# Kernel optimization log

Measured on AMD Instinct MI355X. Metric: run time of the kernel, lower is better.

## Reference

```python
import jax, jax.numpy as jnp
import numpy as np

B, S, D, H, DFF = 2, 2048, 1024, 16, 4096
DK = D // H
EPS = 1e-6
MASK_FILL = -1.0  # original code uses -1**9 == -1 (precedence bug), NOT -1e9


def layernorm(x, gamma, beta):
    # original: (x - mean) / (std + eps), std unbiased (torch default ddof=1), scalar gamma/beta
    mean = jnp.mean(x, axis=-1, keepdims=True)
    std = jnp.std(x, axis=-1, keepdims=True, ddof=1)
    return gamma * (x - mean) / (std + EPS) + beta


def setup_inputs() -> dict:
    key = jax.random.key(0)
    ks = jax.random.split(key, 12)
    sc = 0.02
    return {
        "x": jax.random.normal(ks[0], (B, S, D), jnp.float32),
        "src_mask": jnp.ones((B, 1, 1, S), jnp.int32),
        "wq": jax.random.normal(ks[1], (D, D), jnp.float32) * sc,
        "bq": jnp.zeros((D,), jnp.float32),
        "wk": jax.random.normal(ks[2], (D, D), jnp.float32) * sc,
        "bk": jnp.zeros((D,), jnp.float32),
        "wv": jax.random.normal(ks[3], (D, D), jnp.float32) * sc,
        "bv": jnp.zeros((D,), jnp.float32),
        "wo": jax.random.normal(ks[4], (D, D), jnp.float32) * sc,
        "bo": jnp.zeros((D,), jnp.float32),
        "w1": jax.random.normal(ks[5], (D, DFF), jnp.float32) * sc,
        "b1": jnp.zeros((DFF,), jnp.float32),
        "w2": jax.random.normal(ks[6], (DFF, D), jnp.float32) * sc,
        "b2": jnp.zeros((D,), jnp.float32),
        "g1": jnp.ones((), jnp.float32),
        "be1": jnp.zeros((), jnp.float32),
        "g2": jnp.ones((), jnp.float32),
        "be2": jnp.zeros((), jnp.float32),
    }


def reference(x, src_mask, wq, bq, wk, bk, wv, bv, wo, bo,
              w1, b1, w2, b2, g1, be1, g2, be2):
    # --- residual 1: pre-LN self-attention ---
    xn = layernorm(x, g1, be1)
    q = (xn @ wq + bq).reshape(B, S, H, DK).transpose(0, 2, 1, 3)  # [B,H,S,DK]
    k = (xn @ wk + bk).reshape(B, S, H, DK).transpose(0, 2, 1, 3)
    v = (xn @ wv + bv).reshape(B, S, H, DK).transpose(0, 2, 1, 3)
    scores = jnp.einsum('bhqd,bhkd->bhqk', q, k) / jnp.sqrt(jnp.float32(DK))
    scores = jnp.where(src_mask == 0, MASK_FILL, scores)
    attn = jax.nn.softmax(scores, axis=-1)
    ctx = jnp.einsum('bhqk,bhkd->bhqd', attn, v)
    ctx = ctx.transpose(0, 2, 1, 3).reshape(B, S, D)
    attn_out = ctx @ wo + bo
    x = x + attn_out  # dropout is identity in eval

    # --- residual 2: pre-LN feed-forward ---
    xn = layernorm(x, g2, be2)
    h = jax.nn.relu(xn @ w1 + b1)
    ff_out = h @ w2 + b2
    return x + ff_out
```

## Files before the change

kernel.cpp:

```cpp
#include <hip/hip_runtime.h>

typedef unsigned short u16;
typedef __bf16 bf16x8 __attribute__((ext_vector_type(8)));
typedef float f32x4 __attribute__((ext_vector_type(4)));

#define AS1U(p) ((__attribute__((address_space(1))) unsigned int*)(p))
#define AS3U(p) ((__attribute__((address_space(3))) unsigned int*)(p))

__device__ __forceinline__ u16 f2bf(float f) {
  union { float f; unsigned int i; } c; c.f = f;
  return (u16)((c.i + 0x7FFFu + ((c.i >> 16) & 1u)) >> 16);
}
__device__ __forceinline__ u16 f2bf_trunc(float f) {
  union { float f; unsigned int i; } c; c.f = f;
  return (u16)(c.i >> 16);
}

template <int BM, int BN, int BK, int OMODE>
__global__ __launch_bounds__(256) void gemm_bt(
    const u16* __restrict__ A, long lda,
    const u16* __restrict__ B, long ldb,
    void* __restrict__ Cv, long ldc,
    int K, float scale, const float* __restrict__ bias,
    const float* __restrict__ res, long ldres, int relu) {
  constexpr int WN = (BN == 128) ? 64 : 32;
  constexpr int MI = 4, NJ = WN / 16;
  constexpr int KK = BK / 32;
  __shared__ u16 As0[BM * BK], As1[BM * BK];
  __shared__ u16 Bs0[BN * BK], Bs1[BN * BK];
  const int t = threadIdx.x;
  const int w = t >> 6, l = t & 63;
  const int wr = w >> 1, wc = w & 1;
  const int quad = l >> 4, mlo = l & 15;
  const long row0 = (long)blockIdx.x * BM;
  const long col0 = (long)blockIdx.y * BN;

  f32x4 acc[MI][NJ] = {};

  auto stage = [&](u16 (&Ad)[BM * BK], u16 (&Bd)[BN * BK], int k0) {
    if (BK == 32) {
#pragma unroll
      for (int i = 0; i < BM / 64; i++) {
        int s = t + i * 256, r = s >> 2, c = s & 3;
        const u16* g = A + (row0 + r) * lda + k0 + c * 8;
        __builtin_amdgcn_global_load_lds(AS1U(g), AS3U(&Ad[s * 8]), 16, 0, 0);
      }
#pragma unroll
      for (int i = 0; i < BN / 64; i++) {
        int s = t + i * 256, r = s >> 2, c = s & 3;
        const u16* g = B + (col0 + r) * ldb + k0 + c * 8;
        __builtin_amdgcn_global_load_lds(AS1U(g), AS3U(&Bd[s * 8]), 16, 0, 0);
      }
    } else {
#pragma unroll
      for (int i = 0; i < BM / 32; i++) {
        int s = t + i * 256, r = s >> 3, c = s & 7;
        const u16* g = A + (row0 + r) * lda + k0 + (c ^ (r & 7)) * 8;
        __builtin_amdgcn_global_load_lds(AS1U(g), AS3U(&Ad[s * 8]), 16, 0, 0);
      }
#pragma unroll
      for (int i = 0; i < BN / 32; i++) {
        int s = t + i * 256, r = s >> 3, c = s & 7;
        const u16* g = B + (col0 + r) * ldb + k0 + (c ^ (r & 7)) * 8;
        __builtin_amdgcn_global_load_lds(AS1U(g), AS3U(&Bd[s * 8]), 16, 0, 0);
      }
    }
  };
  auto compute = [&](const u16 (&Asr)[BM * BK], const u16 (&Bsr)[BN * BK]) {
#pragma unroll
    for (int kk = 0; kk < KK; kk++) {
      bf16x8 a[MI], b[NJ];
#pragma unroll
      for (int i = 0; i < MI; i++) {
        int r = wr * 64 + i * 16 + mlo;
        a[i] = (BK == 32) ? *(const bf16x8*)&Asr[(r * 4 + quad) * 8]
                          : *(const bf16x8*)&Asr[(r * 8 + ((kk * 4 + quad) ^ (r & 7))) * 8];
      }
#pragma unroll
      for (int j = 0; j < NJ; j++) {
        int r = wc * WN + j * 16 + mlo;
        b[j] = (BK == 32) ? *(const bf16x8*)&Bsr[(r * 4 + quad) * 8]
                          : *(const bf16x8*)&Bsr[(r * 8 + ((kk * 4 + quad) ^ (r & 7))) * 8];
      }
#pragma unroll
      for (int i = 0; i < MI; i++)
#pragma unroll
        for (int j = 0; j < NJ; j++)
          acc[i][j] = __builtin_amdgcn_mfma_f32_16x16x32_bf16(a[i], b[j], acc[i][j], 0, 0, 0);
    }
  };

  stage(As0, Bs0, 0);
  for (int k0 = 0; k0 < K; k0 += 2 * BK) {
    __syncthreads();
    stage(As1, Bs1, k0 + BK);
    compute(As0, Bs0);
    __syncthreads();
    if (k0 + 2 * BK < K) stage(As0, Bs0, k0 + 2 * BK);
    compute(As1, Bs1);
  }

#pragma unroll
  for (int i = 0; i < MI; i++) {
#pragma unroll
    for (int j = 0; j < NJ; j++) {
      const long gn = col0 + wc * WN + j * 16 + mlo;
      const float bv = bias ? bias[gn] : 0.0f;
#pragma unroll
      for (int r = 0; r < 4; r++) {
        const long gm = row0 + wr * 64 + i * 16 + quad * 4 + r;
        float v = acc[i][j][r] * scale + bv;
        if (relu && v < 0.0f) v = 0.0f;
        if (res) v += res[gm * ldres + gn];
        if (OMODE == 0) ((float*)Cv)[gm * ldc + gn] = v;
        else ((u16*)Cv)[gm * ldc + gn] = f2bf(v);
      }
    }
  }
}

__global__ __launch_bounds__(256) void flash_attn(
    const u16* __restrict__ QKV, const u16* __restrict__ VT,
    const int* __restrict__ mask, u16* __restrict__ ctx) {
  __shared__ u16 Ks[2][64 * 64];
  __shared__ u16 Vs[2][64 * 64];
  __shared__ u16 Ps[128 * 64];
  const int t = threadIdx.x;
  const int w = t >> 6, l = t & 63;
  const int quad = l >> 4, mlo = l & 15;
  const int z = blockIdx.z, b = z >> 4, h = z & 15;
  const long q0 = (long)blockIdx.x * 128;
  const u16* Qg = QKV + (long)b * (2048L * 3072) + h * 64;
  const u16* Kg = Qg + 1024;
  const u16* Vg = VT + (long)b * (1024L * 2048) + (long)(h * 64) * 2048;
  const int* mrow = mask + b * 2048;

#pragma unroll
  for (int i = 0; i < 2; i++) {
    int s = t + i * 256, r = s >> 3, c = s & 7;
    __builtin_amdgcn_global_load_lds(AS1U(Kg + (long)r * 3072 + (c ^ (r & 7)) * 8),
                                     AS3U(&Ks[0][s * 8]), 16, 0, 0);
    __builtin_amdgcn_global_load_lds(AS1U(Vg + (long)r * 2048 + (c ^ (r & 7)) * 8),
                                     AS3U(&Vs[0][s * 8]), 16, 0, 0);
  }
  bf16x8 aq[2][2];
#pragma unroll
  for (int i = 0; i < 2; i++)
#pragma unroll
    for (int kk = 0; kk < 2; kk++) {
      const u16* g = Qg + (q0 + w * 32 + i * 16 + mlo) * 3072 + kk * 32 + quad * 8;
      union { uint4 u; bf16x8 v; } c; c.u = *(const uint4*)g;
      aq[i][kk] = c.v;
    }

  f32x4 o[2][5] = {};
  union { u16 s[8]; bf16x8 v; } ones;
#pragma unroll
  for (int e = 0; e < 8; e++) ones.s[e] = 0x3F80;
  const float CS = 0.125f * 1.44269504f;
  const float CM = -1.44269504f;

  for (int it = 0; it < 32; ++it) {
    const int cur = it & 1;
    const int key0 = it * 64;
    __syncthreads();
    if (it + 1 < 32) {
      const int nb = 1 - cur;
      const u16* Kg2 = Kg + (long)(it + 1) * 64 * 3072;
      const u16* Vg2 = Vg + (it + 1) * 64;
#pragma unroll
      for (int i2 = 0; i2 < 2; i2++) {
        int s = t + i2 * 256, r = s >> 3, c = s & 7;
        __builtin_amdgcn_global_load_lds(AS1U(Kg2 + (long)r * 3072 + (c ^ (r & 7)) * 8),
                                         AS3U(&Ks[nb][s * 8]), 16, 0, 0);
        __builtin_amdgcn_global_load_lds(AS1U(Vg2 + (long)r * 2048 + (c ^ (r & 7)) * 8),
                                         AS3U(&Vs[nb][s * 8]), 16, 0, 0);
      }
    }
    int mz[4];
#pragma unroll
    for (int j = 0; j < 4; j++) mz[j] = mrow[key0 + j * 16 + mlo];
    f32x4 sa[2][4] = {};
#pragma unroll
    for (int kk = 0; kk < 2; kk++) {
      bf16x8 bk[4];
#pragma unroll
      for (int j = 0; j < 4; j++) {
        int rr = j * 16 + mlo;
        bk[j] = *(const bf16x8*)&Ks[cur][(rr * 8 + ((kk * 4 + quad) ^ (mlo & 7))) * 8];
      }
#pragma unroll
      for (int i = 0; i < 2; i++)
#pragma unroll
        for (int j = 0; j < 4; j++)
          sa[i][j] = __builtin_amdgcn_mfma_f32_16x16x32_bf16(aq[i][kk], bk[j], sa[i][j], 0, 0, 0);
    }
#pragma unroll
    for (int i = 0; i < 2; i++) {
      const int rbase = w * 32 + i * 16 + quad * 4;
      const int skey = (rbase >> 2) & 7;
#pragma unroll
      for (int j = 0; j < 4; j++) {
        const int col = j * 16 + mlo;
        u16* pp = &Ps[rbase * 64 + (((col >> 3) ^ skey) << 3) + (col & 7)];
#pragma unroll
        for (int r = 0; r < 4; r++) {
          float s = (mz[j] == 0) ? CM : sa[i][j][r] * CS;
          pp[r * 64] = f2bf_trunc(__builtin_amdgcn_exp2f(s));
        }
      }
    }
#pragma unroll
    for (int kk = 0; kk < 2; kk++) {
      bf16x8 ap[2], bv[4];
#pragma unroll
      for (int i = 0; i < 2; i++) {
        const int row = w * 32 + i * 16 + mlo;
        const int skey = (row >> 2) & 7;
        ap[i] = *(const bf16x8*)&Ps[(row * 8 + ((kk * 4 + quad) ^ skey)) * 8];
      }
#pragma unroll
      for (int j = 0; j < 4; j++) {
        int rr = j * 16 + mlo;
        bv[j] = *(const bf16x8*)&Vs[cur][(rr * 8 + ((kk * 4 + quad) ^ (mlo & 7))) * 8];
      }
#pragma unroll
      for (int i = 0; i < 2; i++) {
#pragma unroll
        for (int j = 0; j < 4; j++)
          o[i][j] = __builtin_amdgcn_mfma_f32_16x16x32_bf16(ap[i], bv[j], o[i][j], 0, 0, 0);
        o[i][4] = __builtin_amdgcn_mfma_f32_16x16x32_bf16(ap[i], ones.v, o[i][4], 0, 0, 0);
      }
    }
  }
  u16* cb = ctx + (long)b * (2048L * 1024) + q0 * 1024 + h * 64;
#pragma unroll
  for (int i = 0; i < 2; i++)
#pragma unroll
    for (int r = 0; r < 4; r++) {
      float inv = 1.0f / o[i][4][r];
      int row = w * 32 + i * 16 + quad * 4 + r;
#pragma unroll
      for (int j = 0; j < 4; j++)
        cb[(long)row * 1024 + j * 16 + mlo] = f2bf(o[i][j][r] * inv);
    }
}

__device__ __forceinline__ void ln_row(const float* __restrict__ x, u16* __restrict__ y,
                                       const float* __restrict__ g, const float* __restrict__ b,
                                       long row, float* ss, float* s2) {
  const float* xr = x + row * 1024;
  float v[4];
  float s = 0.f, sq = 0.f;
#pragma unroll
  for (int i = 0; i < 4; i++) {
    float f = xr[threadIdx.x + i * 256];
    v[i] = f; s += f; sq += f * f;
  }
#pragma unroll
  for (int o = 32; o > 0; o >>= 1) { s += __shfl_xor(s, o, 64); sq += __shfl_xor(sq, o, 64); }
  const int w = threadIdx.x >> 6;
  if ((threadIdx.x & 63) == 0) { ss[w] = s; s2[w] = sq; }
  __syncthreads();
  s = ss[0] + ss[1] + ss[2] + ss[3];
  sq = s2[0] + s2[1] + s2[2] + s2[3];
  const float mean = s * (1.0f / 1024.0f);
  float var = (sq - s * mean) * (1.0f / 1023.0f);
  var = fmaxf(var, 0.0f);
  const float sc = g[0] / (sqrtf(var) + 1e-6f);
  const float be = b[0];
#pragma unroll
  for (int i = 0; i < 4; i++)
    y[row * 1024 + threadIdx.x + i * 256] = f2bf((v[i] - mean) * sc + be);
}

__global__ __launch_bounds__(256) void ln_kernel(const float* __restrict__ x, u16* __restrict__ y,
                                                 const float* __restrict__ g, const float* __restrict__ b) {
  __shared__ float ss[4], s2[4];
  ln_row(x, y, g, b, blockIdx.x, ss, s2);
}

__global__ __launch_bounds__(256) void prep_kernel(
    const float* __restrict__ x, const float* __restrict__ g1, const float* __restrict__ be1,
    const float* __restrict__ wq, const float* __restrict__ wk, const float* __restrict__ wv,
    const float* __restrict__ wo, const float* __restrict__ w1, const float* __restrict__ w2,
    const float* __restrict__ bq, const float* __restrict__ bk, const float* __restrict__ bv,
    u16* __restrict__ xnH, u16* __restrict__ WqkvT, u16* __restrict__ woT,
    u16* __restrict__ w1T, u16* __restrict__ w2T, float* __restrict__ biasQKV) {
  __shared__ float tile[32][33];
  __shared__ float ss[4], s2[4];
  const int bid = blockIdx.x;
  if (bid >= 12300) {
    ln_row(x, xnH, g1, be1, bid - 12300, ss, s2);
    return;
  }
  if (bid >= 12288) {
    const int i = (bid - 12288) * 256 + threadIdx.x;
    if (i < 3072) biasQKV[i] = (i < 1024) ? bq[i] : ((i < 2048) ? bk[i - 1024] : bv[i - 2048]);
    return;
  }
  const float* in; u16* out; long ldin, ldo; int ti, tiles_x;
  if (bid < 1024)      { in = wq; out = WqkvT;                     ldin = 1024; ldo = 1024; ti = bid;        tiles_x = 32; }
  else if (bid < 2048) { in = wk; out = WqkvT + (size_t)1024*1024; ldin = 1024; ldo = 1024; ti = bid - 1024; tiles_x = 32; }
  else if (bid < 3072) { in = wv; out = WqkvT + (size_t)2048*1024; ldin = 1024; ldo = 1024; ti = bid - 2048; tiles_x = 32; }
  else if (bid < 4096) { in = wo; out = woT;                       ldin = 1024; ldo = 1024; ti = bid - 3072; tiles_x = 32; }
  else if (bid < 8192) { in = w1; out = w1T;                       ldin = 4096; ldo = 1024; ti = bid - 4096; tiles_x = 128; }
  else                 { in = w2; out = w2T;                       ldin = 1024; ldo = 4096; ti = bid - 8192; tiles_x = 32; }
  const int bx = (ti % tiles_x) * 32, by = (ti / tiles_x) * 32;
  const int tx = threadIdx.x & 31, ty = threadIdx.x >> 5;
#pragma unroll
  for (int i = 0; i < 32; i += 8) tile[ty + i][tx] = in[(long)(by + ty + i) * ldin + bx + tx];
  __syncthreads();
#pragma unroll
  for (int i = 0; i < 32; i += 8)
    out[(long)(bx + ty + i) * ldo + by + tx] = f2bf(tile[tx][ty + i]);
}

__global__ __launch_bounds__(256) void ttrans1(const u16* __restrict__ in, long ldin, long siz,
                                               u16* __restrict__ out, long ldo, long soz) {
  __shared__ u16 tile[32][33];
  const long zi = (long)blockIdx.z * siz, zo = (long)blockIdx.z * soz;
  const int bx = blockIdx.x * 32, by = blockIdx.y * 32;
  const int tx = threadIdx.x & 31, ty = threadIdx.x >> 5;
#pragma unroll
  for (int i = 0; i < 32; i += 8)
    tile[ty + i][tx] = in[zi + (long)(by + ty + i) * ldin + bx + tx];
  __syncthreads();
#pragma unroll
  for (int i = 0; i < 32; i += 8)
    out[zo + (long)(bx + ty + i) * ldo + by + tx] = tile[tx][ty + i];
}

extern "C" void kernel_launch(void* const* d_in, const int* in_sizes, int n_in,
                              void* d_out, int out_size, void* d_ws, size_t ws_size,
                              hipStream_t stream) {
  const float* x   = (const float*)d_in[0];
  const int*   msk = (const int*)d_in[1];
  const float* wq  = (const float*)d_in[2];
  const float* bq  = (const float*)d_in[3];
  const float* wk  = (const float*)d_in[4];
  const float* bk  = (const float*)d_in[5];
  const float* wv  = (const float*)d_in[6];
  const float* bv  = (const float*)d_in[7];
  const float* wo  = (const float*)d_in[8];
  const float* bo  = (const float*)d_in[9];
  const float* w1  = (const float*)d_in[10];
  const float* b1  = (const float*)d_in[11];
  const float* w2  = (const float*)d_in[12];
  const float* b2  = (const float*)d_in[13];
  const float* g1  = (const float*)d_in[14];
  const float* be1 = (const float*)d_in[15];
  const float* g2  = (const float*)d_in[16];
  const float* be2 = (const float*)d_in[17];
  float* out = (float*)d_out;

  char* basep = (char*)d_ws;
  size_t off = 0;
  auto au = [&](size_t nelem) -> u16* {
    u16* r = (u16*)(basep + off);
    off += ((nelem * 2) + 255) & ~(size_t)255;
    return r;
  };
  auto afp = [&](size_t nelem) -> float* {
    float* r = (float*)(basep + off);
    off += ((nelem * 4) + 255) & ~(size_t)255;
    return r;
  };

  u16* xnH  = au((size_t)4096 * 1024);
  u16* QKV  = au((size_t)4096 * 3072);
  u16* VTH  = au((size_t)2 * 1024 * 2048);
  u16* ctxH = au((size_t)4096 * 1024);
  float* x1 = afp((size_t)4096 * 1024);
  u16* hb   = au((size_t)4096 * 4096);
  u16* WqkvT = au((size_t)3072 * 1024);
  u16* woT  = au((size_t)1024 * 1024);
  u16* w1T  = au((size_t)4096 * 1024);
  u16* w2T  = au((size_t)1024 * 4096);
  float* biasQKV = afp(3072);

  const dim3 blk(256);

  prep_kernel<<<16396, blk, 0, stream>>>(x, g1, be1, wq, wk, wv, wo, w1, w2,
                                         bq, bk, bv, xnH, WqkvT, woT, w1T, w2T, biasQKV);

  gemm_bt<128, 128, 32, 2><<<dim3(32, 24), blk, 0, stream>>>(
      xnH, 1024, WqkvT, 1024, QKV, 3072, 1024, 1.0f,
      biasQKV, (const float*)0, 0, 0);

  ttrans1<<<dim3(32, 64, 2), blk, 0, stream>>>(
      QKV + 2048, 3072, (long)2048 * 3072, VTH, 2048, (long)1024 * 2048);

  flash_attn<<<dim3(16, 1, 32), blk, 0, stream>>>(QKV, VTH, msk, ctxH);

  gemm_bt<128, 64, 64, 0><<<dim3(32, 16), blk, 0, stream>>>(
      ctxH, 1024, woT, 1024, x1, 1024, 1024, 1.0f, bo, x, 1024, 0);

  ln_kernel<<<4096, blk, 0, stream>>>(x1, xnH, g2, be2);

  gemm_bt<128, 128, 32, 2><<<dim3(32, 32), blk, 0, stream>>>(
      xnH, 1024, w1T, 1024, hb, 4096, 1024, 1.0f,
      b1, (const float*)0, 0, 1);

  gemm_bt<128, 64, 64, 0><<<dim3(32, 16), blk, 0, stream>>>(
      hb, 4096, w2T, 4096, out, 1024, 4096, 1.0f, b2, x1, 1024, 0);
}
```

Before: 366.5 us.

## Split attention key range across two blocks and combine partial results

The flash attention kernel now splits the 2048 keys into two halves over a new grid dimension. Each block writes unnormalized fp32 output partials and softmax denominators instead of final bf16 context. A new combine kernel sums the two partials, divides by the summed denominators and writes the bf16 context. This doubles the number of attention blocks to improve CU occupancy and latency hiding. In exchange it adds an extra launch and roughly 32 MB of fp32 partial writes and reads, with the partials buffer reusing the FFN hidden buffer.

```diff
diff --git a/kernel.cpp b/kernel.cpp
--- a/kernel.cpp
+++ b/kernel.cpp
@@ -121,7 +121,8 @@
 
 __global__ __launch_bounds__(256) void flash_attn(
     const u16* __restrict__ QKV, const u16* __restrict__ VT,
-    const int* __restrict__ mask, u16* __restrict__ ctx) {
+    const int* __restrict__ mask, float* __restrict__ opart,
+    float* __restrict__ denp) {
   __shared__ u16 Ks[2][64 * 64];
   __shared__ u16 Vs[2][64 * 64];
   __shared__ u16 Ps[128 * 64];
@@ -129,11 +130,12 @@
   const int w = t >> 6, l = t & 63;
   const int quad = l >> 4, mlo = l & 15;
   const int z = blockIdx.z, b = z >> 4, h = z & 15;
+  const int y = blockIdx.y;
   const long q0 = (long)blockIdx.x * 128;
   const u16* Qg = QKV + (long)b * (2048L * 3072) + h * 64;
-  const u16* Kg = Qg + 1024;
-  const u16* Vg = VT + (long)b * (1024L * 2048) + (long)(h * 64) * 2048;
-  const int* mrow = mask + b * 2048;
+  const u16* Kg = Qg + 1024 + (long)y * 1024 * 3072;
+  const u16* Vg = VT + (long)b * (1024L * 2048) + (long)(h * 64) * 2048 + y * 1024;
+  const int* mrow = mask + b * 2048 + y * 1024;
 
 #pragma unroll
   for (int i = 0; i < 2; i++) {
@@ -160,11 +162,11 @@
   const float CS = 0.125f * 1.44269504f;
   const float CM = -1.44269504f;
 
-  for (int it = 0; it < 32; ++it) {
+  for (int it = 0; it < 16; ++it) {
     const int cur = it & 1;
     const int key0 = it * 64;
     __syncthreads();
-    if (it + 1 < 32) {
+    if (it + 1 < 16) {
       const int nb = 1 - cur;
       const u16* Kg2 = Kg + (long)(it + 1) * 64 * 3072;
       const u16* Vg2 = Vg + (it + 1) * 64;
@@ -233,17 +235,32 @@
       }
     }
   }
-  u16* cb = ctx + (long)b * (2048L * 1024) + q0 * 1024 + h * 64;
+  float* ob = opart + ((long)(y * 32 + z)) * (2048L * 64) + q0 * 64;
+  float* db = denp + ((long)(y * 32 + z)) * 2048 + q0;
 #pragma unroll
   for (int i = 0; i < 2; i++)
 #pragma unroll
     for (int r = 0; r < 4; r++) {
-      float inv = 1.0f / o[i][4][r];
-      int row = w * 32 + i * 16 + quad * 4 + r;
+      const int row = w * 32 + i * 16 + quad * 4 + r;
 #pragma unroll
       for (int j = 0; j < 4; j++)
-        cb[(long)row * 1024 + j * 16 + mlo] = f2bf(o[i][j][r] * inv);
-    }
+        ob[(long)row * 64 + j * 16 + mlo] = o[i][j][r];
+      if (mlo == 0) db[row] = o[i][4][r];
+    }
+}
+
+__global__ __launch_bounds__(256) void fcombine(
+    const float* __restrict__ opart, const float* __restrict__ denp,
+    u16* __restrict__ ctx) {
+  const long e = (long)blockIdx.x * 256 + threadIdx.x;
+  const long PL = 32L * 2048 * 64;
+  const float o0 = opart[e], o1 = opart[e + PL];
+  const int z = (int)(e >> 17);
+  const int rem = (int)(e & 131071);
+  const int q = rem >> 6, d = rem & 63;
+  const float dn = denp[(long)z * 2048 + q] + denp[(long)(32 + z) * 2048 + q];
+  const int b = z >> 4, h = z & 15;
+  ctx[(long)b * (2048L * 1024) + (long)q * 1024 + h * 64 + d] = f2bf((o0 + o1) / dn);
 }
 
 __device__ __forceinline__ void ln_row(const float* __restrict__ x, u16* __restrict__ y,
@@ -378,6 +395,8 @@
   u16* w1T  = au((size_t)4096 * 1024);
   u16* w2T  = au((size_t)1024 * 4096);
   float* biasQKV = afp(3072);
+  float* denp = afp((size_t)2 * 32 * 2048);
+  float* opart = (float*)hb;
 
   const dim3 blk(256);
 
@@ -391,7 +410,8 @@
   ttrans1<<<dim3(32, 64, 2), blk, 0, stream>>>(
       QKV + 2048, 3072, (long)2048 * 3072, VTH, 2048, (long)1024 * 2048);
 
-  flash_attn<<<dim3(16, 1, 32), blk, 0, stream>>>(QKV, VTH, msk, ctxH);
+  flash_attn<<<dim3(16, 2, 32), blk, 0, stream>>>(QKV, VTH, msk, opart, denp);
+  fcombine<<<16384, blk, 0, stream>>>(opart, denp, ctxH);
 
   gemm_bt<128, 64, 64, 0><<<dim3(32, 16), blk, 0, stream>>>(
       ctxH, 1024, woT, 1024, x1, 1024, 1024, 1.0f, bo, x, 1024, 0);
```

Result: slower. 380.4 us (+3.8%).
